# Kernel optimization log

Measured on AMD Instinct MI355X. Metric: run time of the kernel, lower is better.

## Reference

```python
import jax, jax.numpy as jnp
import numpy as np

B, T = 256, 100
EMBED = 36
DM = 72          # d_model = 2*embed_size
H, E = 4, 18     # n_heads, head dim
PATCH, STRIDE = 16, 8
SEQ = T + 1      # 101
PN = (SEQ - PATCH) // STRIDE + 2  # 12
DFF = 4 * H * DM                  # 1152
EPS = 1e-4

def _pe(periods, freqs):
    i = jnp.arange(periods + 1, dtype=jnp.float32)[:, None]
    j = jnp.arange(freqs, dtype=jnp.float32)[None, :]
    ang = (np.pi / periods) * (2.0 ** j) * (i - 1.0)
    return jnp.concatenate([jnp.sin(ang), jnp.cos(ang)], axis=1)  # [periods+1, 2*freqs]

def _ln(x, g, b):
    m = x.mean(-1, keepdims=True)
    v = ((x - m) ** 2).mean(-1, keepdims=True)
    return (x - m) / jnp.sqrt(v + 1e-5) * g + b

def _masked_stats(x, mask):
    # mean/std (population) over masked entries per row; 0 when mask empty
    cnt = mask.sum(1, keepdims=True).astype(x.dtype)
    safe = jnp.maximum(cnt, 1.0)
    mean = jnp.where(mask, x, 0.0).sum(1, keepdims=True) / safe
    var = jnp.where(mask, (x - mean) ** 2, 0.0).sum(1, keepdims=True) / safe
    nz = cnt > 0
    return jnp.where(nz, mean, 0.0), jnp.where(nz, jnp.sqrt(var), 0.0)

def _fwd(history, w_nopos, b_nopos, w_wpos, b_wpos, task_emb,
         w_inp, b_inp, wq, bq, wk, bk, wv, bv, wo, bo,
         w_ff1, b_ff1, w_ff2, b_ff2, g1, be1, g2, be2, ge, bee,
         w_outp, b_outp, w_head, b_head, ts, target_ts, task):
    pe_year, pe_month, pe_day, pe_dow = _pe(10, 4), _pe(12, 4), _pe(31, 6), _pe(7, 4)
    yr = ts[:, :, 0]
    dy = jnp.clip(yr[:, -1:] - yr, 0, 10)
    pos = jnp.concatenate([pe_year[dy], pe_month[ts[:, :, 1]], pe_day[ts[:, :, 2]], pe_dow[ts[:, :, 3]]], -1)  # [B,T,36]
    # --- RobustScaler, fully vectorized over batch ---
    x = history                                  # [B,T]
    mean, std = _masked_stats(x, x != 0)
    clipped = jnp.clip(x, 0.0, mean + 2.0 * std)
    mc, sc = _masked_stats(clipped, clipped != 0)
    s = mc + sc + EPS                            # [B,1]
    scale = s[:, :, None]                        # [B,1,1]
    h = jnp.clip(x / s, 0.0, 3.0)[..., None]     # [B,T,1]
    # --- embeddings ---
    e0 = jax.nn.relu(h @ w_nopos + b_nopos)
    e1 = jax.nn.relu(h @ w_wpos + b_wpos) + pos
    hist = jnp.concatenate([e0, e1], -1)         # [B,T,72]
    tt = target_ts.reshape(-1, 1, 5)
    yrq = jnp.clip(yr[:, -1:] - tt[:, :, 0], 0, 10)
    qp = jnp.concatenate([pe_year[yrq], pe_month[tt[:, :, 1]], pe_day[tt[:, :, 2]], pe_dow[tt[:, :, 3]]], -1)[:, 0]
    t = task_emb[task]                           # [B,36]
    tgt = jnp.concatenate([t, t + qp], -1)       # [B,72]
    hist = jnp.concatenate([hist, tgt[:, None, :]], 1)  # [B,101,72]
    # --- PAttnBlock ---
    m = jax.lax.stop_gradient(hist.mean(1, keepdims=True))
    xc = hist - m
    sd = jnp.sqrt(xc.var(1, keepdims=True) + 1e-5)
    xc = (xc / sd).transpose(0, 2, 1)            # [B,72,101]
    xp = jnp.concatenate([xc, jnp.repeat(xc[..., -1:], STRIDE, axis=-1)], -1)  # replication pad -> [B,72,109]
    idx = jnp.arange(PN)[:, None] * STRIDE + jnp.arange(PATCH)[None, :]
    patches = xp[..., idx]                       # [B,72,PN,PATCH]
    z = patches @ w_inp + b_inp                  # [B,72,PN,DM]
    Bd = B * DM
    z = z.reshape(Bd, PN, DM)
    q = (z @ wq + bq).reshape(Bd, PN, H, E)
    k = (z @ wk + bk).reshape(Bd, PN, H, E)
    v = (z @ wv + bv).reshape(Bd, PN, H, E)
    A = jax.nn.softmax(jnp.einsum('blhe,bshe->bhls', q, k) / np.sqrt(E).astype(np.float32), axis=-1)
    o = jnp.einsum('bhls,bshd->blhd', A, v).reshape(Bd, PN, DM)
    z = z + (o @ wo + bo)
    z = _ln(z, g1, be1)
    ff = jax.nn.gelu(z @ w_ff1 + b_ff1, approximate=False) @ w_ff2 + b_ff2
    z = _ln(z + ff, g2, be2)
    z = _ln(z, ge, bee)                          # encoder final norm
    z = z.reshape(B, DM, PN * DM)
    out0 = (z @ w_outp + b_outp).transpose(0, 2, 1)   # [B,1,72]
    y = jax.nn.relu(out0 @ w_head + b_head)[..., 0]   # [B,1]
    y = (y * scale[:, :, 0])[:, 0]                    # [B]
    return y, scale

def setup_inputs() -> dict:
    key = jax.random.key(0)
    ks = jax.random.split(key, 20)
    def n(k, shape, s=0.05):
        return jax.random.normal(k, shape, jnp.float32) * s
    inp = {
        'history': jax.random.uniform(ks[0], (B, T), jnp.float32),
        'w_nopos': n(ks[1], (1, EMBED)), 'b_nopos': jnp.zeros((EMBED,), jnp.float32),
        'w_wpos': n(ks[2], (1, EMBED)), 'b_wpos': jnp.zeros((EMBED,), jnp.float32),
        'task_emb': n(ks[3], (10, EMBED), 1.0),
        'w_inp': n(ks[4], (PATCH, DM)), 'b_inp': jnp.zeros((DM,), jnp.float32),
        'wq': n(ks[5], (DM, DM)), 'bq': jnp.zeros((DM,), jnp.float32),
        'wk': n(ks[6], (DM, DM)), 'bk': jnp.zeros((DM,), jnp.float32),
        'wv': n(ks[7], (DM, DM)), 'bv': jnp.zeros((DM,), jnp.float32),
        'wo': n(ks[8], (DM, DM)), 'bo': jnp.zeros((DM,), jnp.float32),
        'w_ff1': n(ks[9], (DM, DFF)), 'b_ff1': jnp.zeros((DFF,), jnp.float32),
        'w_ff2': n(ks[10], (DFF, DM)), 'b_ff2': jnp.zeros((DM,), jnp.float32),
        'g1': jnp.ones((DM,), jnp.float32), 'be1': jnp.zeros((DM,), jnp.float32),
        'g2': jnp.ones((DM,), jnp.float32), 'be2': jnp.zeros((DM,), jnp.float32),
        'ge': jnp.ones((DM,), jnp.float32), 'bee': jnp.zeros((DM,), jnp.float32),
        'w_outp': n(ks[11], (PN * DM, 1)), 'b_outp': jnp.zeros((1,), jnp.float32),
        'w_head': n(ks[12], (DM, 1)), 'b_head': jnp.zeros((1,), jnp.float32),
        'ts': jax.random.randint(ks[13], (B, T, 4), 0, 8),
        'target_ts': jax.random.randint(ks[14], (B, 5), 0, 8),
        'task': jax.random.randint(ks[15], (B,), 0, 10),
    }
    return inp

def reference(history, w_nopos, b_nopos, w_wpos, b_wpos, task_emb,
              w_inp, b_inp, wq, bq, wk, bk, wv, bv, wo, bo,
              w_ff1, b_ff1, w_ff2, b_ff2, g1, be1, g2, be2, ge, bee,
              w_outp, b_outp, w_head, b_head, ts, target_ts, task):
    return _fwd(history, w_nopos, b_nopos, w_wpos, b_wpos, task_emb,
                w_inp, b_inp, wq, bq, wk, bk, wv, bv, wo, bo,
                w_ff1, b_ff1, w_ff2, b_ff2, g1, be1, g2, be2, ge, bee,
                w_outp, b_outp, w_head, b_head, ts, target_ts, task)
```

## Files before the change

### kernel.cpp

```cpp
#include <hip/hip_runtime.h>
#include <hip/hip_bf16.h>

#define B_ 256
#define T_ 100
#define EMBED_ 36
#define DM_ 72
#define H_ 4
#define E_ 18
#define PATCH_ 16
#define STRIDE_ 8
#define SEQ_ 101
#define PN_ 12
#define DFF_ 1152

#define KP 96

#define VT2_OFF 18432
#define PT2_OFF 28224
#define OL2_OFF 30528

typedef __attribute__((ext_vector_type(8))) short s8v;
typedef __attribute__((ext_vector_type(4))) float f32x4;

__device__ __forceinline__ unsigned short f2b(float x) {
  __hip_bfloat16 b = __float2bfloat16(x);
  return __builtin_bit_cast(unsigned short, b);
}
__device__ __forceinline__ unsigned short f2bc(float x) {
  return (unsigned short)((__builtin_bit_cast(unsigned int, x) + 0x8000u) >> 16);
}
__device__ __forceinline__ unsigned int pk2f(float lo, float hi) {
  unsigned int ul = __builtin_bit_cast(unsigned int, lo) + 0x8000u;
  unsigned int uh = __builtin_bit_cast(unsigned int, hi) + 0x8000u;
  return __builtin_amdgcn_perm(uh, ul, 0x07060302u);
}
__device__ __forceinline__ s8v zfrag_global(const float* __restrict__ row, int k0) {
  if (k0 >= 72) {
    uint4 z = {0u, 0u, 0u, 0u};
    if (k0 == 72) z.x = 0x3F80u;
    return __builtin_bit_cast(s8v, z);
  }
  float4 f0 = *(const float4*)(row + k0);
  float4 f1 = *(const float4*)(row + k0 + 4);
  uint4 u;
  u.x = pk2f(f0.x, f0.y); u.y = pk2f(f0.z, f0.w);
  u.z = pk2f(f1.x, f1.y); u.w = pk2f(f1.z, f1.w);
  return __builtin_bit_cast(s8v, u);
}

__device__ __forceinline__ float fast_gelu(float x) {
  float u = x * __builtin_fmaf(0.1029437f, x * x, 2.3022085f);
  float e = exp2f(-u);
  return x * __builtin_amdgcn_rcpf(1.0f + e);
}


__device__ __forceinline__ float block_sum1k(float v, float* redw, float* bcast) {
  const int tid = threadIdx.x;
  #pragma unroll
  for (int m = 32; m > 0; m >>= 1) v += __shfl_xor(v, m, 64);
  if ((tid & 63) == 0) redw[tid >> 6] = v;
  __syncthreads();
  if (tid < 16) {
    float r = redw[tid];
    #pragma unroll
    for (int m = 8; m > 0; m >>= 1) r += __shfl_xor(r, m, 64);
    if (tid == 0) *bcast = r;
  }
  __syncthreads();
  float out = *bcast;
  __syncthreads();
  return out;
}

__device__ __forceinline__ float pe_val(float periods, int freqs, int idx, int c) {
  int f = (c < freqs) ? c : (c - freqs);
  float ang = 3.14159265358979323846f / periods * exp2f((float)f) * ((float)idx - 1.0f);
  return (c < freqs) ? sinf(ang) : cosf(ang);
}

__device__ __forceinline__ float pos_feat(int jj, int dy, int mo, int da, int dw) {
  if (jj < 8)  return pe_val(10.f, 4, dy, jj);
  if (jj < 16) return pe_val(12.f, 4, mo, jj - 8);
  if (jj < 28) return pe_val(31.f, 6, da, jj - 16);
  return pe_val(7.f, 4, dw, jj - 28);
}

__global__ __launch_bounds__(1024) void prep_kernel(
    const float* __restrict__ history,
    const float* __restrict__ w_nopos, const float* __restrict__ b_nopos,
    const float* __restrict__ w_wpos, const float* __restrict__ b_wpos,
    const float* __restrict__ task_emb,
    const float* __restrict__ w_inp, const float* __restrict__ b_inp,
    const int* __restrict__ ts, const int* __restrict__ target_ts,
    const int* __restrict__ task,
    const float* __restrict__ wq, const float* __restrict__ wk,
    const float* __restrict__ wvp, const float* __restrict__ wo,
    const float* __restrict__ w1, const float* __restrict__ w2,
    const float* __restrict__ bq, const float* __restrict__ bk,
    const float* __restrict__ bv, const float* __restrict__ bo,
    const float* __restrict__ b1,
    unsigned short* __restrict__ wqkvT, unsigned short* __restrict__ woT,
    unsigned short* __restrict__ w1T, unsigned short* __restrict__ w2P,
    float* __restrict__ zbuf, float* __restrict__ sbuf, float* __restrict__ d_out)
{
  if (blockIdx.x < 228) {
    const float s18 = 0.23570226039551584f;
    int idx = blockIdx.x * 1024 + threadIdx.x;
    if (idx < 23040) {
      int n = idx / 96, k = idx % 96;
      int mat = n / 80, nc = n % 80;
      const float* w = (mat == 0) ? wq : (mat == 1) ? wk : wvp;
      const float* bb = (mat == 0) ? bq : (mat == 1) ? bk : bv;
      float scale = (mat == 0) ? s18 : 1.0f;
      unsigned short v = 0;
      if (nc < 72) {
        if (k < 72) v = f2b(w[k * 72 + nc] * scale);
        else if (k == 72) v = f2b(bb[nc] * scale);
      }
      wqkvT[idx] = v;
    } else if (idx < 30720) {
      int i = idx - 23040;
      int n = i / 96, k = i % 96;
      unsigned short v = 0;
      if (n < 72) {
        if (k < 72) v = f2b(wo[k * 72 + n]);
        else if (k == 72) v = f2b(bo[n]);
      }
      woT[i] = v;
    } else if (idx < 141312) {
      int i = idx - 30720;
      int n = i / 96, k = i % 96;
      unsigned short v = 0;
      if (k < 72) v = f2b(w1[(size_t)k * DFF_ + n]);
      else if (k == 72) v = f2b(b1[n]);
      w1T[i] = v;
    } else if (idx < 233472) {
      int i = idx - 141312;
      int slot = i & 7;
      int lane = (i >> 3) & 63;
      int c    = (i >> 9) % 36;
      int mt5  = i / 18432;
      int la = lane & 15, lg = lane >> 4;
      int kl = (slot < 4) ? (4 * lg + slot) : (16 + 4 * lg + (slot - 4));
      int dff = c * 32 + kl;
      int j = mt5 * 16 + la;
      w2P[i] = (j < 72) ? f2b(w2[(size_t)dff * 72 + j]) : (unsigned short)0;
    }
    return;
  }

  const int b = blockIdx.x - 228, tid = threadIdx.x;
  __shared__ float hs[SEQ_][73];
  __shared__ float redw[16];
  __shared__ float bcast;
  __shared__ float ps1[8][73], ps2[8][73];
  __shared__ float mu[DM_], rsd[DM_];

  const float* x = history + (size_t)b * T_;

  float xv = (tid < T_) ? x[tid] : 0.0f;
  bool msk1 = (tid < T_) && (xv != 0.0f);
  float sum1 = block_sum1k(msk1 ? xv : 0.0f, redw, &bcast);
  float cnt1 = block_sum1k(msk1 ? 1.0f : 0.0f, redw, &bcast);
  float safe1 = fmaxf(cnt1, 1.0f);
  float mean1 = sum1 / safe1;
  float var1 = block_sum1k(msk1 ? (xv - mean1) * (xv - mean1) : 0.0f, redw, &bcast) / safe1;
  float std1 = (cnt1 > 0.f) ? sqrtf(var1) : 0.0f;
  float mn1  = (cnt1 > 0.f) ? mean1 : 0.0f;
  float hi = mn1 + 2.0f * std1;
  float cl = (tid < T_) ? fminf(fmaxf(xv, 0.0f), hi) : 0.0f;

  bool msk2 = (tid < T_) && (cl != 0.0f);
  float sum2 = block_sum1k(msk2 ? cl : 0.0f, redw, &bcast);
  float cnt2 = block_sum1k(msk2 ? 1.0f : 0.0f, redw, &bcast);
  float safe2 = fmaxf(cnt2, 1.0f);
  float mean2 = sum2 / safe2;
  float var2 = block_sum1k(msk2 ? (cl - mean2) * (cl - mean2) : 0.0f, redw, &bcast) / safe2;
  float std2 = (cnt2 > 0.f) ? sqrtf(var2) : 0.0f;
  float mn2  = (cnt2 > 0.f) ? mean2 : 0.0f;
  const float s = mn2 + std2 + 1e-4f;
  if (tid == 0) { sbuf[b] = s; d_out[B_ + b] = s; }

  const int yr_last = ts[((size_t)b * T_ + (T_ - 1)) * 4 + 0];

  for (int o = tid; o < T_ * DM_; o += 1024) {
    int t = o / DM_, j = o % DM_;
    float h = fminf(fmaxf(x[t] / s, 0.0f), 3.0f);
    float val;
    if (j < EMBED_) {
      val = fmaxf(h * w_nopos[j] + b_nopos[j], 0.0f);
    } else {
      int jj = j - EMBED_;
      float e1 = fmaxf(h * w_wpos[jj] + b_wpos[jj], 0.0f);
      const int* tr = ts + ((size_t)b * T_ + t) * 4;
      int dy = min(max(yr_last - tr[0], 0), 10);
      val = e1 + pos_feat(jj, dy, tr[1], tr[2], tr[3]);
    }
    hs[t][j] = val;
  }
  if (tid < DM_) {
    int j = tid;
    float te = task_emb[task[b] * EMBED_ + (j < EMBED_ ? j : j - EMBED_)];
    if (j < EMBED_) {
      hs[T_][j] = te;
    } else {
      int jj = j - EMBED_;
      const int* qr = target_ts + (size_t)b * 5;
      int yq = min(max(yr_last - qr[0], 0), 10);
      hs[T_][j] = te + pos_feat(jj, yq, qr[1], qr[2], qr[3]);
    }
  }
  __syncthreads();

  if (tid < 576) {
    int d = tid % 72, c = tid / 72;
    int t0 = c * 13, t1 = min(t0 + 13, SEQ_);
    float a1 = 0.f, a2 = 0.f;
    for (int t = t0; t < t1; t++) { float v = hs[t][d]; a1 += v; a2 += v * v; }
    ps1[c][d] = a1; ps2[c][d] = a2;
  }
  __syncthreads();
  if (tid < DM_) {
    float S1 = 0.f, S2 = 0.f;
    #pragma unroll
    for (int c = 0; c < 8; c++) { S1 += ps1[c][tid]; S2 += ps2[c][tid]; }
    float m = S1 * (1.0f / (float)SEQ_);
    float v = fmaxf(S2 * (1.0f / (float)SEQ_) - m * m, 0.f);
    mu[tid] = m; rsd[tid] = rsqrtf(v + 1e-5f);
  }
  __syncthreads();
  for (int o = tid; o < SEQ_ * DM_; o += 1024) {
    int t = o / DM_, d = o % DM_;
    hs[t][d] = (hs[t][d] - mu[d]) * rsd[d];
  }
  __syncthreads();

  for (int o4 = tid; o4 < DM_ * PN_ * (DM_ / 4); o4 += 1024) {
    int jg = o4 % 18, p = (o4 / 18) % PN_, d = o4 / (18 * PN_);
    float4 acc = *(const float4*)&b_inp[jg * 4];
    #pragma unroll
    for (int i = 0; i < PATCH_; i++) {
      int t = p * STRIDE_ + i;
      if (t > T_) t = T_;
      float hv = hs[t][d];
      float4 w4 = *(const float4*)&w_inp[i * DM_ + jg * 4];
      acc.x += hv * w4.x; acc.y += hv * w4.y; acc.z += hv * w4.z; acc.w += hv * w4.w;
    }
    *(float4*)&zbuf[((size_t)(b * DM_ + d) * PN_ + p) * DM_ + jg * 4] = acc;
  }
}

__global__ __launch_bounds__(384) void attn_kernel(
    const unsigned short* __restrict__ wqkvT, const unsigned short* __restrict__ woT,
    const float* __restrict__ g1, const float* __restrict__ be1,
    float* __restrict__ zf)
{
  __shared__ __attribute__((aligned(16))) unsigned short AS[38288];

  const int tid = threadIdx.x;
  const int lane = tid & 63, wid = tid >> 6;
  const int m0 = wid * 16;
  const int la = lane & 15, lg = lane >> 4;
  float* zg = zf + (size_t)blockIdx.x * 8 * PN_ * DM_;

  const f32x4 Z4 = {0.f, 0.f, 0.f, 0.f};
  const uint4 ZU = {0u, 0u, 0u, 0u};
  const s8v ZF = __builtin_bit_cast(s8v, ZU);

  for (int i = tid; i < 768; i += 384) {
    int bofs = i * 24 + 18;
    *(unsigned int*)&AS[bofs] = 0u; *(unsigned int*)&AS[bofs + 2] = 0u;
    *(unsigned int*)&AS[bofs + 4] = 0u;
  }
  for (int i = tid; i < 576; i += 384) {
    int h = i / 144, rem = i % 144, e = rem / 8, r = rem % 8;
    int bofs = VT2_OFF + h * 2448 + e * 136 + r * 16 + 12;
    *(unsigned int*)&AS[bofs] = 0u; *(unsigned int*)&AS[bofs + 2] = 0u;
  }
  for (int i = tid; i < 72; i += 384) {
    int bofs = VT2_OFF + (i / 18) * 2448 + (i % 18) * 136 + 128;
    *(unsigned int*)&AS[bofs] = 0u; *(unsigned int*)&AS[bofs + 2] = 0u;
    *(unsigned int*)&AS[bofs + 4] = 0u; *(unsigned int*)&AS[bofs + 6] = 0u;
  }
  for (int i = tid; i < 1152; i += 384)
    ((unsigned int*)&AS[PT2_OFF])[i] = 0u;
  for (int i = tid; i < 96; i += 384) {
    int bofs = OL2_OFF + i * 80 + 72;
    *(unsigned int*)&AS[bofs] = 0x3F80u;
    *(unsigned int*)&AS[bofs + 2] = 0u; *(unsigned int*)&AS[bofs + 4] = 0u;
    *(unsigned int*)&AS[bofs + 6] = 0u;
  }
  for (int i = tid; i < 40; i += 384)
    ((unsigned int*)&AS[OL2_OFF + 96 * 80])[i] = 0u;

  {
    s8v A[3];
    #pragma unroll
    for (int kc = 0; kc < 3; kc++)
      A[kc] = zfrag_global(zg + (m0 + la) * 72, kc * 32 + 8 * lg);

    for (int n0 = 0; n0 < 15; n0++) {
      const int ng = n0 * 16 + la;
      const int mat = ng / 80, nc = ng % 80;
      const int hh = nc / 18, ee = nc % 18;
      f32x4 acc = Z4;
      #pragma unroll
      for (int kc = 0; kc < 3; kc++) {
        s8v Bf = *(const s8v*)&wqkvT[(size_t)ng * KP + kc * 32 + 8 * lg];
        acc = __builtin_amdgcn_mfma_f32_16x16x32_bf16(A[kc], Bf, acc, 0, 0, 0);
      }
      if (nc < 72) {
        if (mat < 2) {
          const int base = ((mat * 4 + hh) * 96) * 24 + ee;
          #pragma unroll
          for (int r = 0; r < 4; r++)
            AS[base + (m0 + 4 * lg + r) * 24] = f2bc(acc[r]);
        } else {
          const int basev = VT2_OFF + hh * 2448 + ee * 136;
          #pragma unroll
          for (int r = 0; r < 4; r++) {
            int tok = m0 + 4 * lg + r;
            AS[basev + (tok / 12) * 16 + tok % 12] = f2bc(acc[r]);
          }
        }
      }
    }
  }
  __syncthreads();

  {
    const float LOG2E = 1.4426950408889634f;
    const int ptb = PT2_OFF + wid * 384;
    for (int u = wid; u < 32; u += 6) {
      const int rg = u >> 2, h = u & 3;
      const int tokb = rg * 12;
      s8v Aq = *(const s8v*)&AS[((0 * 4 + h) * 96 + tokb + la) * 24 + 8 * lg];
      s8v Bk = *(const s8v*)&AS[((1 * 4 + h) * 96 + tokb + la) * 24 + 8 * lg];
      if (lg == 3) { Aq = ZF; Bk = ZF; }
      f32x4 S = __builtin_amdgcn_mfma_f32_16x16x32_bf16(Aq, Bk, Z4, 0, 0, 0);

      float p[4], rcs[4];
      #pragma unroll
      for (int rr = 0; rr < 4; rr++) {
        float t = (la < 12) ? S[rr] : -3.0e38f;
        float mx = t;
        mx = fmaxf(mx, __shfl_xor(mx, 1, 64));
        mx = fmaxf(mx, __shfl_xor(mx, 2, 64));
        mx = fmaxf(mx, __shfl_xor(mx, 4, 64));
        mx = fmaxf(mx, __shfl_xor(mx, 8, 64));
        float pe = exp2f((t - mx) * LOG2E);
        float sm = pe;
        sm += __shfl_xor(sm, 1, 64);
        sm += __shfl_xor(sm, 2, 64);
        sm += __shfl_xor(sm, 4, 64);
        sm += __shfl_xor(sm, 8, 64);
        p[rr] = pe;
        rcs[rr] = __builtin_amdgcn_rcpf(sm);
      }
      #pragma unroll
      for (int rr = 0; rr < 4; rr++)
        AS[ptb + (4 * lg + rr) * 24 + la] = f2bc(p[rr] * rcs[rr]);

      s8v Ap = *(const s8v*)&AS[ptb + la * 24 + 8 * lg];
      if (lg == 3) Ap = ZF;
      s8v Bv0 = *(const s8v*)&AS[VT2_OFF + h * 2448 + la * 136 + rg * 16 + 8 * lg];
      f32x4 O0 = __builtin_amdgcn_mfma_f32_16x16x32_bf16(Ap, Bv0, Z4, 0, 0, 0);
      s8v Bv1 = *(const s8v*)&AS[VT2_OFF + h * 2448 + (16 + la) * 136 + rg * 16 + 8 * lg];
      f32x4 O1 = __builtin_amdgcn_mfma_f32_16x16x32_bf16(Ap, Bv1, Z4, 0, 0, 0);

      if (lg < 3) {
        #pragma unroll
        for (int rr = 0; rr < 4; rr++) {
          int l = 4 * lg + rr;
          AS[OL2_OFF + (tokb + l) * 80 + h * 18 + la] = f2bc(O0[rr]);
          if (la < 2)
            AS[OL2_OFF + (tokb + l) * 80 + h * 18 + 16 + la] = f2bc(O1[rr]);
        }
      }
    }
  }
  __syncthreads();

  {
    s8v A[3];
    #pragma unroll
    for (int kc = 0; kc < 3; kc++)
      A[kc] = *(const s8v*)&AS[OL2_OFF + (m0 + la) * 80 + kc * 32 + 8 * lg];

    f32x4 acc[5];
    #pragma unroll
    for (int n0 = 0; n0 < 5; n0++) {
      acc[n0] = Z4;
      #pragma unroll
      for (int kc = 0; kc < 3; kc++) {
        s8v Bf = *(const s8v*)&woT[(size_t)(n0 * 16 + la) * KP + kc * 32 + 8 * lg];
        acc[n0] = __builtin_amdgcn_mfma_f32_16x16x32_bf16(A[kc], Bf, acc[n0], 0, 0, 0);
      }
    }

    const float inv72 = 1.0f / 72.0f;
    float g1v[5], be1v[5];
    #pragma unroll
    for (int n0 = 0; n0 < 5; n0++) {
      bool ok = (n0 < 4) || (la < 8);
      g1v[n0]  = ok ? g1[n0 * 16 + la] : 0.f;
      be1v[n0] = ok ? be1[n0 * 16 + la] : 0.f;
    }
    #pragma unroll
    for (int r = 0; r < 4; r++) {
      const int t = m0 + 4 * lg + r;
      float vals[5];
      float s1 = 0.f, s2 = 0.f;
      #pragma unroll
      for (int n0 = 0; n0 < 5; n0++) {
        bool ok = (n0 < 4) || (la < 8);
        float x = ok ? (acc[n0][r] + zg[t * 72 + n0 * 16 + la]) : 0.f;
        vals[n0] = x; s1 += x; s2 += x * x;
      }
      s1 += __shfl_xor(s1, 1, 64); s1 += __shfl_xor(s1, 2, 64);
      s1 += __shfl_xor(s1, 4, 64); s1 += __shfl_xor(s1, 8, 64);
      s2 += __shfl_xor(s2, 1, 64); s2 += __shfl_xor(s2, 2, 64);
      s2 += __shfl_xor(s2, 4, 64); s2 += __shfl_xor(s2, 8, 64);
      float mean = s1 * inv72;
      float rs = rsqrtf(fmaxf(s2 * inv72 - mean * mean, 0.f) + 1e-5f);
      #pragma unroll
      for (int n0 = 0; n0 < 5; n0++)
        if ((n0 < 4) || (la < 8))
          zg[t * 72 + n0 * 16 + la] = (vals[n0] - mean) * rs * g1v[n0] + be1v[n0];
    }
  }
}

__global__ __launch_bounds__(128) void ff_kernel(
    const unsigned short* __restrict__ w1T, const unsigned short* __restrict__ w2P,
    const float* __restrict__ b2,
    const float* __restrict__ g2p, const float* __restrict__ be2,
    const float* __restrict__ gep, const float* __restrict__ beep,
    float* __restrict__ zf)
{
  const int tid = threadIdx.x;
  const int lane = tid & 63, wid = tid >> 6;
  const int la = lane & 15, lg = lane >> 4;
  const int tb = wid * 48;
  float* zg = zf + (size_t)blockIdx.x * 96 * DM_;

  const f32x4 Z4 = {0.f, 0.f, 0.f, 0.f};

  s8v Z[3][3];
  #pragma unroll
  for (int nt = 0; nt < 3; nt++)
    #pragma unroll
    for (int kc = 0; kc < 3; kc++)
      Z[nt][kc] = zfrag_global(zg + (tb + nt * 16 + la) * 72, kc * 32 + 8 * lg);

  f32x4 acc2[5][3];
  #pragma unroll
  for (int mt = 0; mt < 5; mt++) {
    f32x4 binit = Z4;
    if (mt < 4 || lg < 2) {
      float bb[4];
      *(float4*)bb = *(const float4*)&b2[mt * 16 + 4 * lg];
      binit[0] = bb[0]; binit[1] = bb[1]; binit[2] = bb[2]; binit[3] = bb[3];
    }
    #pragma unroll
    for (int nt = 0; nt < 3; nt++) acc2[mt][nt] = binit;
  }

  const int w1l = la * 96 + 8 * lg;
  const int w2l = lane * 8;

  s8v Af[6], A2r[5];
  #pragma unroll
  for (int mt = 0; mt < 2; mt++)
    #pragma unroll
    for (int kc = 0; kc < 3; kc++)
      Af[mt * 3 + kc] = *(const s8v*)&w1T[mt * 1536 + kc * 32 + w1l];
  #pragma unroll
  for (int mt = 0; mt < 5; mt++)
    A2r[mt] = *(const s8v*)&w2P[mt * 18432 + w2l];

  for (int c = 0; c < 36; c++) {
    const int cn = (c + 1 < 36) ? c + 1 : 35;
    const int n3072 = cn * 3072, n512 = cn * 512;

    f32x4 D1[2][3];
    #pragma unroll
    for (int mt = 0; mt < 2; mt++)
      #pragma unroll
      for (int nt = 0; nt < 3; nt++) D1[mt][nt] = Z4;
    #pragma unroll
    for (int mt = 0; mt < 2; mt++)
      #pragma unroll
      for (int kc = 0; kc < 3; kc++)
        #pragma unroll
        for (int nt = 0; nt < 3; nt++)
          D1[mt][nt] = __builtin_amdgcn_mfma_f32_16x16x32_bf16(Af[mt * 3 + kc], Z[nt][kc], D1[mt][nt], 0, 0, 0);

    #pragma unroll
    for (int mt = 0; mt < 2; mt++)
      #pragma unroll
      for (int kc = 0; kc < 3; kc++)
        Af[mt * 3 + kc] = *(const s8v*)&w1T[n3072 + mt * 1536 + kc * 32 + w1l];

    s8v B2[3];
    #pragma unroll
    for (int nt = 0; nt < 3; nt++) {
      uint4 u;
      u.x = pk2f(fast_gelu(D1[0][nt][0]), fast_gelu(D1[0][nt][1]));
      u.y = pk2f(fast_gelu(D1[0][nt][2]), fast_gelu(D1[0][nt][3]));
      u.z = pk2f(fast_gelu(D1[1][nt][0]), fast_gelu(D1[1][nt][1]));
      u.w = pk2f(fast_gelu(D1[1][nt][2]), fast_gelu(D1[1][nt][3]));
      B2[nt] = __builtin_bit_cast(s8v, u);
    }

    #pragma unroll
    for (int mt = 0; mt < 5; mt++)
      #pragma unroll
      for (int nt = 0; nt < 3; nt++)
        acc2[mt][nt] = __builtin_amdgcn_mfma_f32_16x16x32_bf16(A2r[mt], B2[nt], acc2[mt][nt], 0, 0, 0);

    #pragma unroll
    for (int mt = 0; mt < 5; mt++)
      A2r[mt] = *(const s8v*)&w2P[mt * 18432 + n512 + w2l];
  }

  const float inv72 = 1.0f / 72.0f;
  #pragma unroll
  for (int nt = 0; nt < 3; nt++) {
    const int t = tb + nt * 16 + la;
    float v[5][4];
    float s1 = 0.f, s2 = 0.f;
    #pragma unroll
    for (int mt = 0; mt < 5; mt++) {
      if (mt < 4 || lg < 2) {
        float rr[4];
        *(float4*)rr = *(const float4*)&zg[t * 72 + mt * 16 + 4 * lg];
        #pragma unroll
        for (int r = 0; r < 4; r++) {
          float x = acc2[mt][nt][r] + rr[r];
          v[mt][r] = x; s1 += x; s2 += x * x;
        }
      } else {
        #pragma unroll
        for (int r = 0; r < 4; r++) v[mt][r] = 0.f;
      }
    }
    s1 += __shfl_xor(s1, 16, 64); s1 += __shfl_xor(s1, 32, 64);
    s2 += __shfl_xor(s2, 16, 64); s2 += __shfl_xor(s2, 32, 64);
    float mean = s1 * inv72;
    float rs = rsqrtf(fmaxf(s2 * inv72 - mean * mean, 0.f) + 1e-5f);

    float w[5][4];
    float t1 = 0.f, t2 = 0.f;
    #pragma unroll
    for (int mt = 0; mt < 5; mt++) {
      if (mt < 4 || lg < 2) {
        float gg[4], bb[4];
        *(float4*)gg = *(const float4*)&g2p[mt * 16 + 4 * lg];
        *(float4*)bb = *(const float4*)&be2[mt * 16 + 4 * lg];
        #pragma unroll
        for (int r = 0; r < 4; r++) {
          float x = (v[mt][r] - mean) * rs * gg[r] + bb[r];
          w[mt][r] = x; t1 += x; t2 += x * x;
        }
      } else {
        #pragma unroll
        for (int r = 0; r < 4; r++) w[mt][r] = 0.f;
      }
    }
    t1 += __shfl_xor(t1, 16, 64); t1 += __shfl_xor(t1, 32, 64);
    t2 += __shfl_xor(t2, 16, 64); t2 += __shfl_xor(t2, 32, 64);
    float m2 = t1 * inv72;
    float rs2 = rsqrtf(fmaxf(t2 * inv72 - m2 * m2, 0.f) + 1e-5f);

    #pragma unroll
    for (int mt = 0; mt < 5; mt++) {
      if (mt < 4 || lg < 2) {
        float gg[4], bb[4], o[4];
        *(float4*)gg = *(const float4*)&gep[mt * 16 + 4 * lg];
        *(float4*)bb = *(const float4*)&beep[mt * 16 + 4 * lg];
        #pragma unroll
        for (int r = 0; r < 4; r++)
          o[r] = (w[mt][r] - m2) * rs2 * gg[r] + bb[r];
        *(float4*)&zg[t * 72 + mt * 16 + 4 * lg] = *(const float4*)o;
      }
    }
  }
}

__global__ __launch_bounds__(1024) void final_kernel(
    const float* __restrict__ zbuf,
    const float* __restrict__ w_outp, const float* __restrict__ b_outp,
    const float* __restrict__ w_head, const float* __restrict__ b_head,
    const float* __restrict__ sbuf, float* __restrict__ d_out)
{
  const int b = blockIdx.x, tid = threadIdx.x;
  const int wave = tid >> 6, lane = tid & 63;
  __shared__ float out0[DM_];
  const float* zb = zbuf + (size_t)b * DM_ * (PN_ * DM_);

  for (int d = wave; d < DM_; d += 16) {
    float acc = 0.f;
    for (int e = lane; e < PN_ * DM_; e += 64) acc += zb[(size_t)d * PN_ * DM_ + e] * w_outp[e];
    #pragma unroll
    for (int m = 32; m > 0; m >>= 1) acc += __shfl_xor(acc, m, 64);
    if (lane == 0) out0[d] = acc + b_outp[0];
  }
  __syncthreads();
  if (tid == 0) {
    float acc = b_head[0];
    for (int d = 0; d < DM_; d++) acc += out0[d] * w_head[d];
    d_out[b] = fmaxf(acc, 0.0f) * sbuf[b];
  }
}

extern "C" void kernel_launch(void* const* d_in, const int* in_sizes, int n_in,
                              void* d_out, int out_size, void* d_ws, size_t ws_size,
                              hipStream_t stream) {
  const float* history  = (const float*)d_in[0];
  const float* w_nopos  = (const float*)d_in[1];
  const float* b_nopos  = (const float*)d_in[2];
  const float* w_wpos   = (const float*)d_in[3];
  const float* b_wpos   = (const float*)d_in[4];
  const float* task_emb = (const float*)d_in[5];
  const float* w_inp    = (const float*)d_in[6];
  const float* b_inp    = (const float*)d_in[7];
  const float* wq = (const float*)d_in[8];
  const float* bq = (const float*)d_in[9];
  const float* wk = (const float*)d_in[10];
  const float* bk = (const float*)d_in[11];
  const float* wv = (const float*)d_in[12];
  const float* bv = (const float*)d_in[13];
  const float* wo = (const float*)d_in[14];
  const float* bo = (const float*)d_in[15];
  const float* w_ff1 = (const float*)d_in[16];
  const float* b_ff1 = (const float*)d_in[17];
  const float* w_ff2 = (const float*)d_in[18];
  const float* b_ff2 = (const float*)d_in[19];
  const float* g1  = (const float*)d_in[20];
  const float* be1 = (const float*)d_in[21];
  const float* g2  = (const float*)d_in[22];
  const float* be2 = (const float*)d_in[23];
  const float* ge  = (const float*)d_in[24];
  const float* bee = (const float*)d_in[25];
  const float* w_outp = (const float*)d_in[26];
  const float* b_outp = (const float*)d_in[27];
  const float* w_head = (const float*)d_in[28];
  const float* b_head = (const float*)d_in[29];
  const int* ts        = (const int*)d_in[30];
  const int* target_ts = (const int*)d_in[31];
  const int* task      = (const int*)d_in[32];

  float* out = (float*)d_out;
  char* ws = (char*)d_ws;
  float* zf   = (float*)ws;
  float* sbuf = (float*)(ws + 63700992);
  unsigned short* wqkvT = (unsigned short*)(ws + 63702016);
  unsigned short* woT   = (unsigned short*)(ws + 63748096);
  unsigned short* w1T   = (unsigned short*)(ws + 63763456);
  unsigned short* w2P   = (unsigned short*)(ws + 63984640);

  prep_kernel<<<484, 1024, 0, stream>>>(history, w_nopos, b_nopos, w_wpos, b_wpos,
      task_emb, w_inp, b_inp, ts, target_ts, task,
      wq, wk, wv, wo, w_ff1, w_ff2, bq, bk, bv, bo, b_ff1,
      wqkvT, woT, w1T, w2P, zf, sbuf, out);
  attn_kernel<<<2304, 384, 0, stream>>>(wqkvT, woT, g1, be1, zf);
  ff_kernel<<<2304, 128, 0, stream>>>(w1T, w2P, b_ff2, g2, be2, ge, bee, zf);
  final_kernel<<<B_, 1024, 0, stream>>>(zf, w_outp, b_outp, w_head, b_head, sbuf, out);
}
```

Measured before the change: 388.6 us.

## Double-buffer FFN weight fragments with two-chunk prefetch distance

Result: no change. 386.7 us (-0.5%).

```diff
diff --git a/kernel.cpp b/kernel.cpp
--- a/kernel.cpp
+++ b/kernel.cpp
@@ -470,59 +470,110 @@
   const int w1l = la * 96 + 8 * lg;
   const int w2l = lane * 8;
 
-  s8v Af[6], A2r[5];
+  s8v AfA[6], A2rA[5], AfB[6], A2rB[5];
   #pragma unroll
   for (int mt = 0; mt < 2; mt++)
     #pragma unroll
-    for (int kc = 0; kc < 3; kc++)
-      Af[mt * 3 + kc] = *(const s8v*)&w1T[mt * 1536 + kc * 32 + w1l];
+    for (int kc = 0; kc < 3; kc++) {
+      AfA[mt * 3 + kc] = *(const s8v*)&w1T[0 * 3072 + mt * 1536 + kc * 32 + w1l];
+      AfB[mt * 3 + kc] = *(const s8v*)&w1T[1 * 3072 + mt * 1536 + kc * 32 + w1l];
+    }
   #pragma unroll
-  for (int mt = 0; mt < 5; mt++)
-    A2r[mt] = *(const s8v*)&w2P[mt * 18432 + w2l];
-
-  for (int c = 0; c < 36; c++) {
-    const int cn = (c + 1 < 36) ? c + 1 : 35;
-    const int n3072 = cn * 3072, n512 = cn * 512;
-
-    f32x4 D1[2][3];
-    #pragma unroll
-    for (int mt = 0; mt < 2; mt++)
-      #pragma unroll
-      for (int nt = 0; nt < 3; nt++) D1[mt][nt] = Z4;
-    #pragma unroll
-    for (int mt = 0; mt < 2; mt++)
-      #pragma unroll
-      for (int kc = 0; kc < 3; kc++)
+  for (int mt = 0; mt < 5; mt++) {
+    A2rA[mt] = *(const s8v*)&w2P[mt * 18432 + 0 * 512 + w2l];
+    A2rB[mt] = *(const s8v*)&w2P[mt * 18432 + 1 * 512 + w2l];
+  }
+
+  #pragma unroll 1
+  for (int c = 0; c < 36; c += 2) {
+    {
+      const int cn = (c + 2 < 36) ? c + 2 : 35;
+      const int n3072 = cn * 3072, n512 = cn * 512;
+
+      f32x4 D1[2][3];
+      #pragma unroll
+      for (int mt = 0; mt < 2; mt++)
+        #pragma unroll
+        for (int nt = 0; nt < 3; nt++) D1[mt][nt] = Z4;
+      #pragma unroll
+      for (int mt = 0; mt < 2; mt++)
+        #pragma unroll
+        for (int kc = 0; kc < 3; kc++)
+          #pragma unroll
+          for (int nt = 0; nt < 3; nt++)
+            D1[mt][nt] = __builtin_amdgcn_mfma_f32_16x16x32_bf16(AfA[mt * 3 + kc], Z[nt][kc], D1[mt][nt], 0, 0, 0);
+
+      #pragma unroll
+      for (int mt = 0; mt < 2; mt++)
+        #pragma unroll
+        for (int kc = 0; kc < 3; kc++)
+          AfA[mt * 3 + kc] = *(const s8v*)&w1T[n3072 + mt * 1536 + kc * 32 + w1l];
+
+      s8v B2[3];
+      #pragma unroll
+      for (int nt = 0; nt < 3; nt++) {
+        uint4 u;
+        u.x = pk2f(fast_gelu(D1[0][nt][0]), fast_gelu(D1[0][nt][1]));
+        u.y = pk2f(fast_gelu(D1[0][nt][2]), fast_gelu(D1[0][nt][3]));
+        u.z = pk2f(fast_gelu(D1[1][nt][0]), fast_gelu(D1[1][nt][1]));
+        u.w = pk2f(fast_gelu(D1[1][nt][2]), fast_gelu(D1[1][nt][3]));
+        B2[nt] = __builtin_bit_cast(s8v, u);
+      }
+
+      #pragma unroll
+      for (int mt = 0; mt < 5; mt++)
         #pragma unroll
         for (int nt = 0; nt < 3; nt++)
-          D1[mt][nt] = __builtin_amdgcn_mfma_f32_16x16x32_bf16(Af[mt * 3 + kc], Z[nt][kc], D1[mt][nt], 0, 0, 0);
-
-    #pragma unroll
-    for (int mt = 0; mt < 2; mt++)
-      #pragma unroll
-      for (int kc = 0; kc < 3; kc++)
-        Af[mt * 3 + kc] = *(const s8v*)&w1T[n3072 + mt * 1536 + kc * 32 + w1l];
-
-    s8v B2[3];
-    #pragma unroll
-    for (int nt = 0; nt < 3; nt++) {
-      uint4 u;
-      u.x = pk2f(fast_gelu(D1[0][nt][0]), fast_gelu(D1[0][nt][1]));
-      u.y = pk2f(fast_gelu(D1[0][nt][2]), fast_gelu(D1[0][nt][3]));
-      u.z = pk2f(fast_gelu(D1[1][nt][0]), fast_gelu(D1[1][nt][1]));
-      u.w = pk2f(fast_gelu(D1[1][nt][2]), fast_gelu(D1[1][nt][3]));
-      B2[nt] = __builtin_bit_cast(s8v, u);
-    }
-
-    #pragma unroll
-    for (int mt = 0; mt < 5; mt++)
-      #pragma unroll
-      for (int nt = 0; nt < 3; nt++)
-        acc2[mt][nt] = __builtin_amdgcn_mfma_f32_16x16x32_bf16(A2r[mt], B2[nt], acc2[mt][nt], 0, 0, 0);
-
-    #pragma unroll
-    for (int mt = 0; mt < 5; mt++)
-      A2r[mt] = *(const s8v*)&w2P[mt * 18432 + n512 + w2l];
+          acc2[mt][nt] = __builtin_amdgcn_mfma_f32_16x16x32_bf16(A2rA[mt], B2[nt], acc2[mt][nt], 0, 0, 0);
+
+      #pragma unroll
+      for (int mt = 0; mt < 5; mt++)
+        A2rA[mt] = *(const s8v*)&w2P[mt * 18432 + n512 + w2l];
+    }
+    {
+      const int cn = (c + 3 < 36) ? c + 3 : 35;
+      const int n3072 = cn * 3072, n512 = cn * 512;
+
+      f32x4 D1[2][3];
+      #pragma unroll
+      for (int mt = 0; mt < 2; mt++)
+        #pragma unroll
+        for (int nt = 0; nt < 3; nt++) D1[mt][nt] = Z4;
+      #pragma unroll
+      for (int mt = 0; mt < 2; mt++)
+        #pragma unroll
+        for (int kc = 0; kc < 3; kc++)
+          #pragma unroll
+          for (int nt = 0; nt < 3; nt++)
+            D1[mt][nt] = __builtin_amdgcn_mfma_f32_16x16x32_bf16(AfB[mt * 3 + kc], Z[nt][kc], D1[mt][nt], 0, 0, 0);
+
+      #pragma unroll
+      for (int mt = 0; mt < 2; mt++)
+        #pragma unroll
+        for (int kc = 0; kc < 3; kc++)
+          AfB[mt * 3 + kc] = *(const s8v*)&w1T[n3072 + mt * 1536 + kc * 32 + w1l];
+
+      s8v B2[3];
+      #pragma unroll
+      for (int nt = 0; nt < 3; nt++) {
+        uint4 u;
+        u.x = pk2f(fast_gelu(D1[0][nt][0]), fast_gelu(D1[0][nt][1]));
+        u.y = pk2f(fast_gelu(D1[0][nt][2]), fast_gelu(D1[0][nt][3]));
+        u.z = pk2f(fast_gelu(D1[1][nt][0]), fast_gelu(D1[1][nt][1]));
+        u.w = pk2f(fast_gelu(D1[1][nt][2]), fast_gelu(D1[1][nt][3]));
+        B2[nt] = __builtin_bit_cast(s8v, u);
+      }
+
+      #pragma unroll
+      for (int mt = 0; mt < 5; mt++)
+        #pragma unroll
+        for (int nt = 0; nt < 3; nt++)
+          acc2[mt][nt] = __builtin_amdgcn_mfma_f32_16x16x32_bf16(A2rB[mt], B2[nt], acc2[mt][nt], 0, 0, 0);
+
+      #pragma unroll
+      for (int mt = 0; mt < 5; mt++)
+        A2rB[mt] = *(const s8v*)&w2P[mt * 18432 + n512 + w2l];
+    }
   }
 
   const float inv72 = 1.0f / 72.0f;
```

## Split FF hidden dimension across two wave pairs with LDS reduction

Applied to the files above, without the earlier changes.

Result: faster. 378.0 us (-2.7%).

```diff
diff --git a/kernel.cpp b/kernel.cpp
--- a/kernel.cpp
+++ b/kernel.cpp
@@ -432,17 +432,21 @@
   }
 }
 
-__global__ __launch_bounds__(128) void ff_kernel(
+__global__ __launch_bounds__(256) void ff_kernel(
     const unsigned short* __restrict__ w1T, const unsigned short* __restrict__ w2P,
     const float* __restrict__ b2,
     const float* __restrict__ g2p, const float* __restrict__ be2,
     const float* __restrict__ gep, const float* __restrict__ beep,
     float* __restrict__ zf)
 {
+  __shared__ float accl[128 * 61];
+
   const int tid = threadIdx.x;
   const int lane = tid & 63, wid = tid >> 6;
+  const int wsub = wid & 1;
+  const int ch   = wid >> 1;
   const int la = lane & 15, lg = lane >> 4;
-  const int tb = wid * 48;
+  const int tb = wsub * 48;
   float* zg = zf + (size_t)blockIdx.x * 96 * DM_;
 
   const f32x4 Z4 = {0.f, 0.f, 0.f, 0.f};
@@ -458,7 +462,7 @@
   #pragma unroll
   for (int mt = 0; mt < 5; mt++) {
     f32x4 binit = Z4;
-    if (mt < 4 || lg < 2) {
+    if (ch == 0 && (mt < 4 || lg < 2)) {
       float bb[4];
       *(float4*)bb = *(const float4*)&b2[mt * 16 + 4 * lg];
       binit[0] = bb[0]; binit[1] = bb[1]; binit[2] = bb[2]; binit[3] = bb[3];
@@ -469,19 +473,20 @@
 
   const int w1l = la * 96 + 8 * lg;
   const int w2l = lane * 8;
+  const int c0 = ch * 18, c1 = c0 + 18;
 
   s8v Af[6], A2r[5];
   #pragma unroll
   for (int mt = 0; mt < 2; mt++)
     #pragma unroll
     for (int kc = 0; kc < 3; kc++)
-      Af[mt * 3 + kc] = *(const s8v*)&w1T[mt * 1536 + kc * 32 + w1l];
+      Af[mt * 3 + kc] = *(const s8v*)&w1T[c0 * 3072 + mt * 1536 + kc * 32 + w1l];
   #pragma unroll
   for (int mt = 0; mt < 5; mt++)
-    A2r[mt] = *(const s8v*)&w2P[mt * 18432 + w2l];
-
-  for (int c = 0; c < 36; c++) {
-    const int cn = (c + 1 < 36) ? c + 1 : 35;
+    A2r[mt] = *(const s8v*)&w2P[mt * 18432 + c0 * 512 + w2l];
+
+  for (int c = c0; c < c1; c++) {
+    const int cn = (c + 1 < c1) ? c + 1 : c1 - 1;
     const int n3072 = cn * 3072, n512 = cn * 512;
 
     f32x4 D1[2][3];
@@ -525,65 +530,87 @@
       A2r[mt] = *(const s8v*)&w2P[mt * 18432 + n512 + w2l];
   }
 
-  const float inv72 = 1.0f / 72.0f;
-  #pragma unroll
-  for (int nt = 0; nt < 3; nt++) {
-    const int t = tb + nt * 16 + la;
-    float v[5][4];
-    float s1 = 0.f, s2 = 0.f;
-    #pragma unroll
-    for (int mt = 0; mt < 5; mt++) {
-      if (mt < 4 || lg < 2) {
-        float rr[4];
-        *(float4*)rr = *(const float4*)&zg[t * 72 + mt * 16 + 4 * lg];
-        #pragma unroll
-        for (int r = 0; r < 4; r++) {
-          float x = acc2[mt][nt][r] + rr[r];
-          v[mt][r] = x; s1 += x; s2 += x * x;
-        }
-      } else {
-        #pragma unroll
-        for (int r = 0; r < 4; r++) v[mt][r] = 0.f;
-      }
-    }
-    s1 += __shfl_xor(s1, 16, 64); s1 += __shfl_xor(s1, 32, 64);
-    s2 += __shfl_xor(s2, 16, 64); s2 += __shfl_xor(s2, 32, 64);
-    float mean = s1 * inv72;
-    float rs = rsqrtf(fmaxf(s2 * inv72 - mean * mean, 0.f) + 1e-5f);
-
-    float w[5][4];
-    float t1 = 0.f, t2 = 0.f;
-    #pragma unroll
-    for (int mt = 0; mt < 5; mt++) {
-      if (mt < 4 || lg < 2) {
-        float gg[4], bb[4];
-        *(float4*)gg = *(const float4*)&g2p[mt * 16 + 4 * lg];
-        *(float4*)bb = *(const float4*)&be2[mt * 16 + 4 * lg];
-        #pragma unroll
-        for (int r = 0; r < 4; r++) {
-          float x = (v[mt][r] - mean) * rs * gg[r] + bb[r];
-          w[mt][r] = x; t1 += x; t2 += x * x;
-        }
-      } else {
-        #pragma unroll
-        for (int r = 0; r < 4; r++) w[mt][r] = 0.f;
-      }
-    }
-    t1 += __shfl_xor(t1, 16, 64); t1 += __shfl_xor(t1, 32, 64);
-    t2 += __shfl_xor(t2, 16, 64); t2 += __shfl_xor(t2, 32, 64);
-    float m2 = t1 * inv72;
-    float rs2 = rsqrtf(fmaxf(t2 * inv72 - m2 * m2, 0.f) + 1e-5f);
-
-    #pragma unroll
-    for (int mt = 0; mt < 5; mt++) {
-      if (mt < 4 || lg < 2) {
-        float gg[4], bb[4], o[4];
-        *(float4*)gg = *(const float4*)&gep[mt * 16 + 4 * lg];
-        *(float4*)bb = *(const float4*)&beep[mt * 16 + 4 * lg];
+  if (wid >= 2) {
+    float* dst = &accl[(tid - 128) * 61];
+    #pragma unroll
+    for (int mt = 0; mt < 5; mt++)
+      #pragma unroll
+      for (int nt = 0; nt < 3; nt++)
         #pragma unroll
         for (int r = 0; r < 4; r++)
-          o[r] = (w[mt][r] - m2) * rs2 * gg[r] + bb[r];
-        *(float4*)&zg[t * 72 + mt * 16 + 4 * lg] = *(const float4*)o;
+          dst[(mt * 3 + nt) * 4 + r] = acc2[mt][nt][r];
+  }
+  __syncthreads();
+  if (wid < 2) {
+    const float* src = &accl[tid * 61];
+    #pragma unroll
+    for (int mt = 0; mt < 5; mt++)
+      #pragma unroll
+      for (int nt = 0; nt < 3; nt++)
+        #pragma unroll
+        for (int r = 0; r < 4; r++)
+          acc2[mt][nt][r] += src[(mt * 3 + nt) * 4 + r];
+
+    const float inv72 = 1.0f / 72.0f;
+    #pragma unroll
+    for (int nt = 0; nt < 3; nt++) {
+      const int t = tb + nt * 16 + la;
+      float v[5][4];
+      float s1 = 0.f, s2 = 0.f;
+      #pragma unroll
+      for (int mt = 0; mt < 5; mt++) {
+        if (mt < 4 || lg < 2) {
+          float rr[4];
+          *(float4*)rr = *(const float4*)&zg[t * 72 + mt * 16 + 4 * lg];
+          #pragma unroll
+          for (int r = 0; r < 4; r++) {
+            float x = acc2[mt][nt][r] + rr[r];
+            v[mt][r] = x; s1 += x; s2 += x * x;
+          }
+        } else {
+          #pragma unroll
+          for (int r = 0; r < 4; r++) v[mt][r] = 0.f;
+        }
+      }
+      s1 += __shfl_xor(s1, 16, 64); s1 += __shfl_xor(s1, 32, 64);
+      s2 += __shfl_xor(s2, 16, 64); s2 += __shfl_xor(s2, 32, 64);
+      float mean = s1 * inv72;
+      float rs = rsqrtf(fmaxf(s2 * inv72 - mean * mean, 0.f) + 1e-5f);
+
+      float w[5][4];
+      float t1 = 0.f, t2 = 0.f;
+      #pragma unroll
+      for (int mt = 0; mt < 5; mt++) {
+        if (mt < 4 || lg < 2) {
+          float gg[4], bb[4];
+          *(float4*)gg = *(const float4*)&g2p[mt * 16 + 4 * lg];
+          *(float4*)bb = *(const float4*)&be2[mt * 16 + 4 * lg];
+          #pragma unroll
+          for (int r = 0; r < 4; r++) {
+            float x = (v[mt][r] - mean) * rs * gg[r] + bb[r];
+            w[mt][r] = x; t1 += x; t2 += x * x;
+          }
+        } else {
+          #pragma unroll
+          for (int r = 0; r < 4; r++) w[mt][r] = 0.f;
+        }
+      }
+      t1 += __shfl_xor(t1, 16, 64); t1 += __shfl_xor(t1, 32, 64);
+      t2 += __shfl_xor(t2, 16, 64); t2 += __shfl_xor(t2, 32, 64);
+      float m2 = t1 * inv72;
+      float rs2 = rsqrtf(fmaxf(t2 * inv72 - m2 * m2, 0.f) + 1e-5f);
+
+      #pragma unroll
+      for (int mt = 0; mt < 5; mt++) {
+        if (mt < 4 || lg < 2) {
+          float gg[4], bb[4], o[4];
+          *(float4*)gg = *(const float4*)&gep[mt * 16 + 4 * lg];
+          *(float4*)bb = *(const float4*)&beep[mt * 16 + 4 * lg];
+          #pragma unroll
+          for (int r = 0; r < 4; r++)
+            o[r] = (w[mt][r] - m2) * rs2 * gg[r] + bb[r];
+          *(float4*)&zg[t * 72 + mt * 16 + 4 * lg] = *(const float4*)o;
+        }
       }
     }
   }
@@ -666,6 +693,6 @@
       wq, wk, wv, wo, w_ff1, w_ff2, bq, bk, bv, bo, b_ff1,
       wqkvT, woT, w1T, w2P, zf, sbuf, out);
   attn_kernel<<<2304, 384, 0, stream>>>(wqkvT, woT, g1, be1, zf);
-  ff_kernel<<<2304, 128, 0, stream>>>(w1T, w2P, b_ff2, g2, be2, ge, bee, zf);
+  ff_kernel<<<2304, 256, 0, stream>>>(w1T, w2P, b_ff2, g2, be2, ge, bee, zf);
   final_kernel<<<B_, 1024, 0, stream>>>(zf, w_outp, b_outp, w_head, b_head, sbuf, out);
 }
```
